# Kernel tuning notes

Measured on AMD Instinct MI355X. Metric: run time of the kernel, lower is better.

## Reference

```python
import jax, jax.numpy as jnp
import numpy as np

HIDDEN = 1024
HEADS = 16
HEAD = HIDDEN // HEADS
B, S = 2, 2048


def setup_inputs() -> dict:
    key = jax.random.key(0)
    ks = jax.random.split(key, 8)
    query = jax.random.normal(ks[0], (B, S, HIDDEN), dtype=jnp.float32)
    key_t = jax.random.normal(ks[1], (B, S, HIDDEN), dtype=jnp.float32)
    value = jax.random.normal(ks[2], (B, S, HIDDEN), dtype=jnp.float32)
    # causal mask, broadcastable over batch and heads; 0 -> masked (-inf)
    mask = jnp.tril(jnp.ones((S, S), dtype=jnp.int32))[None, None, :, :]
    # torch Linear weights are [out_features, in_features]
    scale = 0.02
    Wq = jax.random.normal(ks[3], (HIDDEN, HIDDEN), dtype=jnp.float32) * scale
    Wk = jax.random.normal(ks[4], (HIDDEN, HIDDEN), dtype=jnp.float32) * scale
    Wv = jax.random.normal(ks[5], (HIDDEN, HIDDEN), dtype=jnp.float32) * scale
    Wo = jax.random.normal(ks[6], (HIDDEN, HIDDEN), dtype=jnp.float32) * scale
    bo = jax.random.normal(ks[7], (HIDDEN,), dtype=jnp.float32) * scale
    return {"query": query, "key": key_t, "value": value, "mask": mask,
            "Wq": Wq, "Wk": Wk, "Wv": Wv, "Wo": Wo, "bo": bo}


def reference(query, key, value, mask, Wq, Wk, Wv, Wo, bo):
    b = query.shape[0]
    # Linear (no bias): x @ W^T, then split into heads -> [b, h, s, d]
    def heads(x, W):
        y = jnp.einsum('bse,oe->bso', x, W)
        return y.reshape(b, -1, HEADS, HEAD).transpose(0, 2, 1, 3)
    Q = heads(query, Wq)
    K = heads(key, Wk)
    V = heads(value, Wv)
    inv_scale = 1.0 / jnp.sqrt(jnp.float32(HEAD))
    scores = jnp.einsum('bhqd,bhkd->bhqk', Q, K) * inv_scale  # [b,h,s,s]
    scores = jnp.where(mask == 0, -jnp.inf, scores)
    attn = jax.nn.softmax(scores, axis=-1)
    x = jnp.einsum('bhqk,bhkd->bhqd', attn, V)
    x = x.transpose(0, 2, 1, 3).reshape(b, -1, HIDDEN)
    return jnp.einsum('bse,oe->bso', x, Wo) + bo
```

## Files before the change

### kernel.cpp

```cpp
#include <hip/hip_runtime.h>


typedef __attribute__((ext_vector_type(8))) short short8;
typedef __attribute__((ext_vector_type(4))) short short4_;
typedef __attribute__((ext_vector_type(4))) float f32x4;
typedef unsigned int u32;
typedef unsigned short u16;

__device__ inline f32x4 mfma16(short8 a, short8 b, f32x4 c) {
    return __builtin_amdgcn_mfma_f32_16x16x32_bf16(a, b, c, 0, 0, 0);
}
__device__ inline u16 f2bf(float f) {
    union { float f; u32 u; } v; v.f = f;
    u32 r = v.u + 0x7fff + ((v.u >> 16) & 1);
    return (u16)(r >> 16);
}
__device__ inline void gll16(void* lds, const void* g) {
    __builtin_amdgcn_global_load_lds((const __attribute__((address_space(1))) u32*)g,
                                     (__attribute__((address_space(3))) u32*)lds,
                                     16, 0, 0);
}

__global__ __launch_bounds__(256)
void cvt_all(const float* __restrict__ q, const float* __restrict__ k,
             const float* __restrict__ v, const float* __restrict__ wq,
             const float* __restrict__ wk, const float* __restrict__ wv,
             const float* __restrict__ wo,
             u16* __restrict__ q16, u16* __restrict__ k16,
             u16* __restrict__ v16, u16* __restrict__ w16) {
    const size_t QKV = 1u << 22;
    const size_t WSZ = 1u << 20;
    size_t base = ((size_t)blockIdx.x * 256 + threadIdx.x) * 8;
    const float* src; u16* dst; size_t off; float scale = 1.0f;
    if (base < QKV)            { src = q; dst = q16; off = base;           scale = 0.125f; }
    else if (base < 2 * QKV)   { src = k; dst = k16; off = base - QKV;     }
    else if (base < 3 * QKV)   { src = v; dst = v16; off = base - 2 * QKV; }
    else {
        size_t wb = base - 3 * QKV;
        int wi = (int)(wb >> 20); off = wb & (WSZ - 1);
        src = wi == 0 ? wq : wi == 1 ? wk : wi == 2 ? wv : wo;
        dst = w16 + (size_t)wi * WSZ;
    }
    float4 f0 = *(const float4*)(src + off);
    float4 f1 = *(const float4*)(src + off + 4);
    short8 s = { (short)f2bf(f0.x * scale), (short)f2bf(f0.y * scale),
                 (short)f2bf(f0.z * scale), (short)f2bf(f0.w * scale),
                 (short)f2bf(f1.x * scale), (short)f2bf(f1.y * scale),
                 (short)f2bf(f1.z * scale), (short)f2bf(f1.w * scale) };
    *(short8*)(dst + off) = s;
}

__global__ __launch_bounds__(256)
void gemm_qkv(const u16* __restrict__ q16, const u16* __restrict__ k16,
              const u16* __restrict__ v16, const u16* __restrict__ w16,
              u16* __restrict__ Qg, u16* __restrict__ Kg, u16* __restrict__ Vt) {
    const int K = 1024;
    __shared__ u16 As[128 * 64];
    __shared__ u16 Bs[128 * 64];
    const int z = blockIdx.z;
    const u16* A = z == 0 ? q16 : z == 1 ? k16 : v16;
    const u16* W = w16 + (size_t)z * (1u << 20);

    const int tid = threadIdx.x, lane = tid & 63, w = tid >> 6;
    const int ln15 = lane & 15, quad = lane >> 4;
    const int lr = lane >> 3, lc = (lane & 7) * 8;
    const int m0 = blockIdx.y * 128, n0 = blockIdx.x * 128;
    const int wm = (w >> 1) * 64, wn = (w & 1) * 64;

    f32x4 acc[4][4] = {};

    for (int k0 = 0; k0 < K; k0 += 64) {
        #pragma unroll
        for (int c = 0; c < 4; ++c) {
            gll16(&As[(w * 32 + c * 8) * 64],
                  &A[(size_t)(m0 + w * 32 + c * 8 + lr) * K + k0 + lc]);
            gll16(&Bs[(w * 32 + c * 8) * 64],
                  &W[(size_t)(n0 + w * 32 + c * 8 + lr) * K + k0 + lc]);
        }
        __syncthreads();
        #pragma unroll
        for (int kh = 0; kh < 2; ++kh) {
            short8 a[4], b[4];
            #pragma unroll
            for (int mt = 0; mt < 4; ++mt)
                a[mt] = *(const short8*)&As[(wm + mt * 16 + ln15) * 64 + kh * 32 + quad * 8];
            #pragma unroll
            for (int nt = 0; nt < 4; ++nt)
                b[nt] = *(const short8*)&Bs[(wn + nt * 16 + ln15) * 64 + kh * 32 + quad * 8];
            #pragma unroll
            for (int mt = 0; mt < 4; ++mt)
                #pragma unroll
                for (int nt = 0; nt < 4; ++nt)
                    acc[mt][nt] = mfma16(a[mt], b[nt], acc[mt][nt]);
        }
        __syncthreads();
    }

    #pragma unroll
    for (int mt = 0; mt < 4; ++mt)
        #pragma unroll
        for (int nt = 0; nt < 4; ++nt)
            #pragma unroll
            for (int r = 0; r < 4; ++r) {
                int m = m0 + wm + mt * 16 + quad * 4 + r;
                int n = n0 + wn + nt * 16 + ln15;
                u16 hv = f2bf(acc[mt][nt][r]);
                if (z == 2) {
                    int b_ = m >> 11, s_ = m & 2047, h_ = n >> 6, d_ = n & 63;
                    int kl = s_ & 63;
                    int sp = (s_ & ~63) + (kl & 15) * 4 + (kl >> 4);
                    Vt[((size_t)(b_ * 16 + h_) * 64 + d_) * 2048 + sp] = hv;
                } else {
                    u16* dst = z ? Kg : Qg;
                    dst[(size_t)m * 1024 + n] = hv;
                }
            }
}

__global__ __launch_bounds__(256)
void gemm_out(const u16* __restrict__ A, const u16* __restrict__ W,
              const float* __restrict__ bias, float* __restrict__ out) {
    const int K = 1024;
    __shared__ u16 As[128 * 64];
    __shared__ u16 Bs[128 * 64];
    const int tid = threadIdx.x, lane = tid & 63, w = tid >> 6;
    const int ln15 = lane & 15, quad = lane >> 4;
    const int lr = lane >> 3, lc = (lane & 7) * 8;
    const int m0 = blockIdx.y * 128, n0 = blockIdx.x * 128;
    const int wm = (w >> 1) * 64, wn = (w & 1) * 64;

    f32x4 acc[4][4] = {};

    for (int k0 = 0; k0 < K; k0 += 64) {
        #pragma unroll
        for (int c = 0; c < 4; ++c) {
            gll16(&As[(w * 32 + c * 8) * 64],
                  &A[(size_t)(m0 + w * 32 + c * 8 + lr) * K + k0 + lc]);
            gll16(&Bs[(w * 32 + c * 8) * 64],
                  &W[(size_t)(n0 + w * 32 + c * 8 + lr) * K + k0 + lc]);
        }
        __syncthreads();
        #pragma unroll
        for (int kh = 0; kh < 2; ++kh) {
            short8 a[4], b[4];
            #pragma unroll
            for (int mt = 0; mt < 4; ++mt)
                a[mt] = *(const short8*)&As[(wm + mt * 16 + ln15) * 64 + kh * 32 + quad * 8];
            #pragma unroll
            for (int nt = 0; nt < 4; ++nt)
                b[nt] = *(const short8*)&Bs[(wn + nt * 16 + ln15) * 64 + kh * 32 + quad * 8];
            #pragma unroll
            for (int mt = 0; mt < 4; ++mt)
                #pragma unroll
                for (int nt = 0; nt < 4; ++nt)
                    acc[mt][nt] = mfma16(a[mt], b[nt], acc[mt][nt]);
        }
        __syncthreads();
    }

    #pragma unroll
    for (int mt = 0; mt < 4; ++mt)
        #pragma unroll
        for (int nt = 0; nt < 4; ++nt)
            #pragma unroll
            for (int r = 0; r < 4; ++r) {
                int m = m0 + wm + mt * 16 + quad * 4 + r;
                int n = n0 + wn + nt * 16 + ln15;
                out[(size_t)m * 1024 + n] = acc[mt][nt][r] + bias[n];
            }
}

__global__ __launch_bounds__(256)
void attn3(const u16* __restrict__ Qg, const u16* __restrict__ Kg,
           const u16* __restrict__ Vt, u16* __restrict__ Xb) {
    __shared__ u16 Kl[2][64 * 64];
    __shared__ u16 Vl[2][64 * 64];
    __shared__ u16 Pl[4][16 * 72];

    const int id = blockIdx.x + 16 * blockIdx.y;
    const int bh = id & 31, qp = id >> 5;
    const int b = bh >> 4, h = bh & 15;
    const int tid = threadIdx.x, lane = tid & 63, w = tid >> 6;
    const int ln15 = lane & 15, quad = lane >> 4;
    const int lr = lane >> 3, lc = (lane & 7) * 8;
    const u16* Kbase = Kg + (size_t)b * 2048 * 1024 + h * 64;
    const u16* Vbase = Vt + (size_t)bh * 64 * 2048;
    const float M0 = 6.0f;

    for (int t = 0; t < 2; ++t) {
        const int qt = t == 0 ? qp : 31 - qp;
        const int q0 = qt * 64;

        const u16* qrow = Qg + (size_t)(b * 2048 + q0 + w * 16 + ln15) * 1024 + h * 64;
        short8 aq0 = *(const short8*)(qrow + quad * 8);
        short8 aq1 = *(const short8*)(qrow + 32 + quad * 8);
        __asm__ volatile("s_waitcnt vmcnt(0)" ::: "memory");

        f32x4 o[4] = {};
        float lsum[4] = {0.f, 0.f, 0.f, 0.f};

        #pragma unroll
        for (int c = 0; c < 2; ++c) {
            const int r0 = w * 16 + c * 8;
            gll16(&Kl[0][r0 * 64], Kbase + (size_t)(0 + r0 + lr) * 1024 + lc);
            gll16(&Vl[0][r0 * 64], Vbase + (size_t)(r0 + lr) * 2048 + 0 + lc);
        }

        for (int kt = 0; kt <= qt; ++kt) {
            const int cur = kt & 1;
            const bool more = kt < qt;
            if (more) {
                const int nb = (kt + 1) & 1, nk = (kt + 1) * 64;
                #pragma unroll
                for (int c = 0; c < 2; ++c) {
                    const int r0 = w * 16 + c * 8;
                    gll16(&Kl[nb][r0 * 64], Kbase + (size_t)(nk + r0 + lr) * 1024 + lc);
                    gll16(&Vl[nb][r0 * 64], Vbase + (size_t)(r0 + lr) * 2048 + nk + lc);
                }
                __asm__ volatile("s_waitcnt vmcnt(4)" ::: "memory");
            } else {
                __asm__ volatile("s_waitcnt vmcnt(0)" ::: "memory");
            }
            __builtin_amdgcn_s_barrier();

            f32x4 sc[4];
            #pragma unroll
            for (int ct = 0; ct < 4; ++ct) {
                short8 b0 = *(const short8*)&Kl[cur][(ct * 16 + ln15) * 64 + quad * 8];
                short8 b1 = *(const short8*)&Kl[cur][(ct * 16 + ln15) * 64 + 32 + quad * 8];
                f32x4 c = {};
                c = mfma16(aq0, b0, c);
                c = mfma16(aq1, b1, c);
                sc[ct] = c;
            }

            const bool diag = (kt == qt);
            #pragma unroll
            for (int r = 0; r < 4; ++r) {
                float s0 = sc[0][r], s1 = sc[1][r], s2 = sc[2][r], s3 = sc[3][r];
                if (diag) {
                    const int qq = w * 16 + quad * 4 + r;
                    s0 = (ln15      <= qq) ? s0 : -1e30f;
                    s1 = (16 + ln15 <= qq) ? s1 : -1e30f;
                    s2 = (32 + ln15 <= qq) ? s2 : -1e30f;
                    s3 = (48 + ln15 <= qq) ? s3 : -1e30f;
                }
                float p0 = __expf(s0 - M0), p1 = __expf(s1 - M0);
                float p2 = __expf(s2 - M0), p3 = __expf(s3 - M0);
                short4_ pw = { (short)f2bf(p0), (short)f2bf(p1),
                               (short)f2bf(p2), (short)f2bf(p3) };
                *(short4_*)&Pl[w][(quad * 4 + r) * 72 + ln15 * 4] = pw;
                lsum[r] += (p0 + p1) + (p2 + p3);
            }

            __asm__ volatile("s_waitcnt lgkmcnt(0)" ::: "memory");
            short8 ap0 = *(const short8*)&Pl[w][ln15 * 72 + quad * 8];
            short8 ap1 = *(const short8*)&Pl[w][ln15 * 72 + 32 + quad * 8];

            #pragma unroll
            for (int dt = 0; dt < 4; ++dt) {
                short8 bv0 = *(const short8*)&Vl[cur][(dt * 16 + ln15) * 64 + quad * 8];
                short8 bv1 = *(const short8*)&Vl[cur][(dt * 16 + ln15) * 64 + 32 + quad * 8];
                o[dt] = mfma16(ap0, bv0, o[dt]);
                o[dt] = mfma16(ap1, bv1, o[dt]);
            }
            __builtin_amdgcn_s_barrier();
        }

        #pragma unroll
        for (int r = 0; r < 4; ++r) {
            float l = lsum[r];
            #pragma unroll
            for (int off = 1; off < 16; off <<= 1)
                l += __shfl_xor(l, off);
            lsum[r] = l;
        }
        #pragma unroll
        for (int dt = 0; dt < 4; ++dt)
            #pragma unroll
            for (int r = 0; r < 4; ++r) {
                int q = q0 + w * 16 + quad * 4 + r;
                Xb[(size_t)(b * 2048 + q) * 1024 + h * 64 + dt * 16 + ln15] =
                    f2bf(o[dt][r] / lsum[r]);
            }
    }
}

extern "C" void kernel_launch(void* const* d_in, const int* in_sizes, int n_in,
                              void* d_out, int out_size, void* d_ws, size_t ws_size,
                              hipStream_t stream) {
    const float* query = (const float*)d_in[0];
    const float* key   = (const float*)d_in[1];
    const float* value = (const float*)d_in[2];
    const float* Wq = (const float*)d_in[4];
    const float* Wk = (const float*)d_in[5];
    const float* Wv = (const float*)d_in[6];
    const float* Wo = (const float*)d_in[7];
    const float* bo = (const float*)d_in[8];
    float* out = (float*)d_out;

    u16* ws  = (u16*)d_ws;
    const size_t T = 1ull << 22;
    u16* q16 = ws;
    u16* k16 = ws + T;
    u16* v16 = ws + 2 * T;
    u16* w16 = ws + 3 * T;
    u16* Qg  = ws + 4 * T;
    u16* Kg  = ws + 5 * T;
    u16* Vt  = (u16*)d_out;
    u16* Xb  = q16;
    const size_t WSZ = 1ull << 20;

    cvt_all<<<8192, 256, 0, stream>>>(query, key, value, Wq, Wk, Wv, Wo,
                                      q16, k16, v16, w16);

    gemm_qkv<<<dim3(8, 32, 3), 256, 0, stream>>>(q16, k16, v16, w16, Qg, Kg, Vt);

    attn3<<<dim3(16, 32), 256, 0, stream>>>(Qg, Kg, Vt, Xb);

    gemm_out<<<dim3(8, 32), 256, 0, stream>>>(Xb, w16 + 3 * WSZ, bo, out);
}
```

Before: 257.7 us.

## Double-buffer GEMM tiles and XOR-swizzle LDS layout in GEMMs and attention

The QKV and output GEMMs now use two LDS buffers, prefetching the next K-tile with global_load_lds while computing on the current one, with explicit vmcnt waits and s_barrier in place of __syncthreads. All three kernels also apply an XOR swizzle to the 16-byte chunk column on the global side (lane^row) and undo it on LDS reads, to reduce LDS bank conflicts on the row-strided short8 reads. LDS use in the GEMMs doubles to 64KB, which may lower occupancy.

New measurement: 238.5 us. 7.4% less time.

```diff
diff --git a/kernel.cpp b/kernel.cpp
--- a/kernel.cpp
+++ b/kernel.cpp
@@ -55,45 +55,64 @@
               const u16* __restrict__ v16, const u16* __restrict__ w16,
               u16* __restrict__ Qg, u16* __restrict__ Kg, u16* __restrict__ Vt) {
     const int K = 1024;
-    __shared__ u16 As[128 * 64];
-    __shared__ u16 Bs[128 * 64];
+    __shared__ u16 As[2][128 * 64];
+    __shared__ u16 Bs[2][128 * 64];
     const int z = blockIdx.z;
     const u16* A = z == 0 ? q16 : z == 1 ? k16 : v16;
     const u16* W = w16 + (size_t)z * (1u << 20);
 
     const int tid = threadIdx.x, lane = tid & 63, w = tid >> 6;
-    const int ln15 = lane & 15, quad = lane >> 4;
-    const int lr = lane >> 3, lc = (lane & 7) * 8;
+    const int ln15 = lane & 15, quad = lane >> 4, s7 = ln15 & 7;
+    const int lr = lane >> 3;
+    const int lcs = (((lane & 7) ^ lr) << 3);
     const int m0 = blockIdx.y * 128, n0 = blockIdx.x * 128;
     const int wm = (w >> 1) * 64, wn = (w & 1) * 64;
 
     f32x4 acc[4][4] = {};
 
-    for (int k0 = 0; k0 < K; k0 += 64) {
-        #pragma unroll
-        for (int c = 0; c < 4; ++c) {
-            gll16(&As[(w * 32 + c * 8) * 64],
-                  &A[(size_t)(m0 + w * 32 + c * 8 + lr) * K + k0 + lc]);
-            gll16(&Bs[(w * 32 + c * 8) * 64],
-                  &W[(size_t)(n0 + w * 32 + c * 8 + lr) * K + k0 + lc]);
-        }
-        __syncthreads();
+    #pragma unroll
+    for (int c = 0; c < 4; ++c) {
+        gll16(&As[0][(w * 32 + c * 8) * 64],
+              &A[(size_t)(m0 + w * 32 + c * 8 + lr) * K + lcs]);
+        gll16(&Bs[0][(w * 32 + c * 8) * 64],
+              &W[(size_t)(n0 + w * 32 + c * 8 + lr) * K + lcs]);
+    }
+
+    for (int i = 0; i < 16; ++i) {
+        const int cur = i & 1;
+        if (i < 15) {
+            const int nb = cur ^ 1, k0 = (i + 1) * 64;
+            #pragma unroll
+            for (int c = 0; c < 4; ++c) {
+                gll16(&As[nb][(w * 32 + c * 8) * 64],
+                      &A[(size_t)(m0 + w * 32 + c * 8 + lr) * K + k0 + lcs]);
+                gll16(&Bs[nb][(w * 32 + c * 8) * 64],
+                      &W[(size_t)(n0 + w * 32 + c * 8 + lr) * K + k0 + lcs]);
+            }
+            __asm__ volatile("s_waitcnt vmcnt(8)" ::: "memory");
+        } else {
+            __asm__ volatile("s_waitcnt vmcnt(0)" ::: "memory");
+        }
+        __builtin_amdgcn_s_barrier();
+
         #pragma unroll
         for (int kh = 0; kh < 2; ++kh) {
             short8 a[4], b[4];
             #pragma unroll
             for (int mt = 0; mt < 4; ++mt)
-                a[mt] = *(const short8*)&As[(wm + mt * 16 + ln15) * 64 + kh * 32 + quad * 8];
+                a[mt] = *(const short8*)&As[cur][(wm + mt * 16 + ln15) * 64 +
+                                                (((kh * 4 + quad) ^ s7) << 3)];
             #pragma unroll
             for (int nt = 0; nt < 4; ++nt)
-                b[nt] = *(const short8*)&Bs[(wn + nt * 16 + ln15) * 64 + kh * 32 + quad * 8];
+                b[nt] = *(const short8*)&Bs[cur][(wn + nt * 16 + ln15) * 64 +
+                                                (((kh * 4 + quad) ^ s7) << 3)];
             #pragma unroll
             for (int mt = 0; mt < 4; ++mt)
                 #pragma unroll
                 for (int nt = 0; nt < 4; ++nt)
                     acc[mt][nt] = mfma16(a[mt], b[nt], acc[mt][nt]);
         }
-        __syncthreads();
+        __builtin_amdgcn_s_barrier();
     }
 
     #pragma unroll
@@ -121,41 +140,60 @@
 void gemm_out(const u16* __restrict__ A, const u16* __restrict__ W,
               const float* __restrict__ bias, float* __restrict__ out) {
     const int K = 1024;
-    __shared__ u16 As[128 * 64];
-    __shared__ u16 Bs[128 * 64];
+    __shared__ u16 As[2][128 * 64];
+    __shared__ u16 Bs[2][128 * 64];
     const int tid = threadIdx.x, lane = tid & 63, w = tid >> 6;
-    const int ln15 = lane & 15, quad = lane >> 4;
-    const int lr = lane >> 3, lc = (lane & 7) * 8;
+    const int ln15 = lane & 15, quad = lane >> 4, s7 = ln15 & 7;
+    const int lr = lane >> 3;
+    const int lcs = (((lane & 7) ^ lr) << 3);
     const int m0 = blockIdx.y * 128, n0 = blockIdx.x * 128;
     const int wm = (w >> 1) * 64, wn = (w & 1) * 64;
 
     f32x4 acc[4][4] = {};
 
-    for (int k0 = 0; k0 < K; k0 += 64) {
-        #pragma unroll
-        for (int c = 0; c < 4; ++c) {
-            gll16(&As[(w * 32 + c * 8) * 64],
-                  &A[(size_t)(m0 + w * 32 + c * 8 + lr) * K + k0 + lc]);
-            gll16(&Bs[(w * 32 + c * 8) * 64],
-                  &W[(size_t)(n0 + w * 32 + c * 8 + lr) * K + k0 + lc]);
-        }
-        __syncthreads();
+    #pragma unroll
+    for (int c = 0; c < 4; ++c) {
+        gll16(&As[0][(w * 32 + c * 8) * 64],
+              &A[(size_t)(m0 + w * 32 + c * 8 + lr) * K + lcs]);
+        gll16(&Bs[0][(w * 32 + c * 8) * 64],
+              &W[(size_t)(n0 + w * 32 + c * 8 + lr) * K + lcs]);
+    }
+
+    for (int i = 0; i < 16; ++i) {
+        const int cur = i & 1;
+        if (i < 15) {
+            const int nb = cur ^ 1, k0 = (i + 1) * 64;
+            #pragma unroll
+            for (int c = 0; c < 4; ++c) {
+                gll16(&As[nb][(w * 32 + c * 8) * 64],
+                      &A[(size_t)(m0 + w * 32 + c * 8 + lr) * K + k0 + lcs]);
+                gll16(&Bs[nb][(w * 32 + c * 8) * 64],
+                      &W[(size_t)(n0 + w * 32 + c * 8 + lr) * K + k0 + lcs]);
+            }
+            __asm__ volatile("s_waitcnt vmcnt(8)" ::: "memory");
+        } else {
+            __asm__ volatile("s_waitcnt vmcnt(0)" ::: "memory");
+        }
+        __builtin_amdgcn_s_barrier();
+
         #pragma unroll
         for (int kh = 0; kh < 2; ++kh) {
             short8 a[4], b[4];
             #pragma unroll
             for (int mt = 0; mt < 4; ++mt)
-                a[mt] = *(const short8*)&As[(wm + mt * 16 + ln15) * 64 + kh * 32 + quad * 8];
+                a[mt] = *(const short8*)&As[cur][(wm + mt * 16 + ln15) * 64 +
+                                                (((kh * 4 + quad) ^ s7) << 3)];
             #pragma unroll
             for (int nt = 0; nt < 4; ++nt)
-                b[nt] = *(const short8*)&Bs[(wn + nt * 16 + ln15) * 64 + kh * 32 + quad * 8];
+                b[nt] = *(const short8*)&Bs[cur][(wn + nt * 16 + ln15) * 64 +
+                                                (((kh * 4 + quad) ^ s7) << 3)];
             #pragma unroll
             for (int mt = 0; mt < 4; ++mt)
                 #pragma unroll
                 for (int nt = 0; nt < 4; ++nt)
                     acc[mt][nt] = mfma16(a[mt], b[nt], acc[mt][nt]);
         }
-        __syncthreads();
+        __builtin_amdgcn_s_barrier();
     }
 
     #pragma unroll
@@ -181,8 +219,9 @@
     const int bh = id & 31, qp = id >> 5;
     const int b = bh >> 4, h = bh & 15;
     const int tid = threadIdx.x, lane = tid & 63, w = tid >> 6;
-    const int ln15 = lane & 15, quad = lane >> 4;
-    const int lr = lane >> 3, lc = (lane & 7) * 8;
+    const int ln15 = lane & 15, quad = lane >> 4, s7 = ln15 & 7;
+    const int lr = lane >> 3;
+    const int lcs = (((lane & 7) ^ lr) << 3);
     const u16* Kbase = Kg + (size_t)b * 2048 * 1024 + h * 64;
     const u16* Vbase = Vt + (size_t)bh * 64 * 2048;
     const float M0 = 6.0f;
@@ -202,20 +241,19 @@
         #pragma unroll
         for (int c = 0; c < 2; ++c) {
             const int r0 = w * 16 + c * 8;
-            gll16(&Kl[0][r0 * 64], Kbase + (size_t)(0 + r0 + lr) * 1024 + lc);
-            gll16(&Vl[0][r0 * 64], Vbase + (size_t)(r0 + lr) * 2048 + 0 + lc);
+            gll16(&Kl[0][r0 * 64], Kbase + (size_t)(r0 + lr) * 1024 + lcs);
+            gll16(&Vl[0][r0 * 64], Vbase + (size_t)(r0 + lr) * 2048 + lcs);
         }
 
         for (int kt = 0; kt <= qt; ++kt) {
             const int cur = kt & 1;
-            const bool more = kt < qt;
-            if (more) {
-                const int nb = (kt + 1) & 1, nk = (kt + 1) * 64;
+            if (kt < qt) {
+                const int nb = cur ^ 1, nk = (kt + 1) * 64;
                 #pragma unroll
                 for (int c = 0; c < 2; ++c) {
                     const int r0 = w * 16 + c * 8;
-                    gll16(&Kl[nb][r0 * 64], Kbase + (size_t)(nk + r0 + lr) * 1024 + lc);
-                    gll16(&Vl[nb][r0 * 64], Vbase + (size_t)(r0 + lr) * 2048 + nk + lc);
+                    gll16(&Kl[nb][r0 * 64], Kbase + (size_t)(nk + r0 + lr) * 1024 + lcs);
+                    gll16(&Vl[nb][r0 * 64], Vbase + (size_t)(r0 + lr) * 2048 + nk + lcs);
                 }
                 __asm__ volatile("s_waitcnt vmcnt(4)" ::: "memory");
             } else {
@@ -226,8 +264,10 @@
             f32x4 sc[4];
             #pragma unroll
             for (int ct = 0; ct < 4; ++ct) {
-                short8 b0 = *(const short8*)&Kl[cur][(ct * 16 + ln15) * 64 + quad * 8];
-                short8 b1 = *(const short8*)&Kl[cur][(ct * 16 + ln15) * 64 + 32 + quad * 8];
+                short8 b0 = *(const short8*)&Kl[cur][(ct * 16 + ln15) * 64 +
+                                                    ((quad ^ s7) << 3)];
+                short8 b1 = *(const short8*)&Kl[cur][(ct * 16 + ln15) * 64 +
+                                                    (((4 + quad) ^ s7) << 3)];
                 f32x4 c = {};
                 c = mfma16(aq0, b0, c);
                 c = mfma16(aq1, b1, c);
@@ -259,8 +299,10 @@
 
             #pragma unroll
             for (int dt = 0; dt < 4; ++dt) {
-                short8 bv0 = *(const short8*)&Vl[cur][(dt * 16 + ln15) * 64 + quad * 8];
-                short8 bv1 = *(const short8*)&Vl[cur][(dt * 16 + ln15) * 64 + 32 + quad * 8];
+                short8 bv0 = *(const short8*)&Vl[cur][(dt * 16 + ln15) * 64 +
+                                                     ((quad ^ s7) << 3)];
+                short8 bv1 = *(const short8*)&Vl[cur][(dt * 16 + ln15) * 64 +
+                                                     (((4 + quad) ^ s7) << 3)];
                 o[dt] = mfma16(ap0, bv0, o[dt]);
                 o[dt] = mfma16(ap1, bv1, o[dt]);
             }
```
